# Kernel optimization log

Hardware: AMD Instinct MI355X
Metric: run time of the kernel (lower is better)

## Reference

```python
import jax, jax.numpy as jnp
import numpy as np

N, E, IN_FEATS, D, H, DIST_DIM, NBOUND = 10000, 160000, 128, 64, 4, 32, 31

def setup_inputs() -> dict:
    key = jax.random.key(0)
    ks = jax.random.split(key, 16)
    gain = 5.0 / 3.0  # tanh gain
    def xavier(k, shape):
        # xavier_normal over the last two dims (fan_in, fan_out) as torch does per-slice
        fan_in, fan_out = shape[-2], shape[-1]
        std = gain * np.sqrt(2.0 / (fan_in + fan_out))
        return jax.random.normal(k, shape, dtype=jnp.float32) * std
    inp = {
        'feat': jax.random.normal(ks[0], (N, IN_FEATS), dtype=jnp.float32),
        'locations': jax.random.normal(ks[1], (N, 3), dtype=jnp.float32),
        'src': jax.random.randint(ks[2], (E,), 0, N),
        'dst': jax.random.randint(ks[3], (E,), 0, N),
        'inter_ids': jax.random.randint(ks[4], (E, H), 0, N),
        'W_fc': xavier(ks[5], (IN_FEATS, H * D)),
        'embed_table': jax.random.normal(ks[6], (NBOUND + 1, DIST_DIM), dtype=jnp.float32),
        'G': xavier(ks[7], (H, DIST_DIM, D)),
        'attn_fc1': xavier(ks[8], (H, 2 * D, D)),
        'attn_fc2': xavier(ks[9], (H, 2 * D, D)),
        'attn_fc3': xavier(ks[10], (H, 2 * D, D)),
        'attn_fc': xavier(ks[11], (H, 3 * D, D)),
        'attn_out': xavier(ks[12], (H, D, 1)),
        'boundaries': jnp.linspace(0.1, 3.1, NBOUND).astype(jnp.float32),
    }
    return inp


def reference(feat, locations, W_fc, embed_table, G, attn_fc1, attn_fc2, attn_fc3,
              attn_fc, attn_out, boundaries, src, dst, inter_ids):
    n = feat.shape[0]
    h = (feat @ W_fc).reshape(n, H, D)                      # [N,H,D]
    pos = locations                                          # [N,3]
    src_pos = pos[src]                                       # [E,3]
    dst_pos = pos[dst]                                       # [E,3]
    inter_pos = pos[inter_ids]                               # [E,H,3]
    h_src = h[src]                                           # [E,H,D]
    h_dst = h[dst]                                           # [E,H,D]
    head_idx = jnp.arange(H)[None, :]
    inter_h = h[inter_ids, head_idx, :]                      # [E,H,D] per-head gather

    e_count = src.shape[0]
    dist1 = jnp.broadcast_to(jnp.linalg.norm(dst_pos - src_pos, axis=-1)[:, None], (e_count, H))
    dist2 = jnp.linalg.norm(dst_pos[:, None, :] - inter_pos, axis=-1)   # [E,H]
    dist_ = jnp.linalg.norm(src_pos[:, None, :] - inter_pos, axis=-1)   # [E,H]

    def dist_embed(dist):
        idx = jnp.searchsorted(boundaries, dist, side='left')  # torch.bucketize(right=False)
        e = embed_table[idx]                                   # [E,H,DIST_DIM]
        return jnp.einsum('ehk,hkd->ehd', e, G)                # [E,H,D]

    de1 = dist_embed(dist1)
    de2 = dist_embed(dist2)
    de_ = dist_embed(dist_)

    d1 = jnp.einsum('ehk,hkd->ehd', jnp.concatenate([h_src, de1], axis=-1), attn_fc1)
    d2 = jnp.einsum('ehk,hkd->ehd', jnp.concatenate([inter_h, de2], axis=-1), attn_fc2)
    d3 = jnp.einsum('ehk,hkd->ehd', jnp.concatenate([h_dst, de_], axis=-1), attn_fc3)

    h_c = jnp.tanh(jnp.einsum('ehk,hkd->ehd', jnp.concatenate([d1, d2, d3], axis=-1), attn_fc))
    e_score = jnp.einsum('ehd,hdo->eho', h_c, attn_out)[..., 0]        # [E,H]

    # edge softmax grouped by destination node
    m = jax.ops.segment_max(e_score, dst, num_segments=n)              # [N,H]
    ex = jnp.exp(e_score - m[dst])
    den = jax.ops.segment_sum(ex, dst, num_segments=n)                 # [N,H]
    a = ex / den[dst]                                                  # [E,H]

    ft = jax.ops.segment_sum(a[:, :, None] * h_src, dst, num_segments=n)  # [N,H,D]
    rst = jnp.mean(ft, axis=1)                                          # merge='mean' -> [N,D]
    return rst
```

## Files before the change

kernel.cpp:

```cpp
#include <hip/hip_runtime.h>
#include <hip/hip_fp16.h>
#include <math.h>

#define N_NODES 10000
#define E_EDGES 160000
#define DMODEL 64
#define H 4
#define NBOUND 31
#define SLOTS 64
#define QREC 1024

typedef _Float16 half8 __attribute__((ext_vector_type(8)));
typedef float floatx4 __attribute__((ext_vector_type(4)));

__device__ __forceinline__ void mm4(const float* __restrict__ S, int aoff,
                                    int astride, int boff, int i0, int j,
                                    int Kdim, float o[4]) {
  float a0 = 0.f, a1 = 0.f, a2 = 0.f, a3 = 0.f;
  for (int t4 = 0; t4 < (Kdim >> 2); ++t4) {
    float4 f0 = *(const float4*)&S[aoff + (i0 + 0) * astride + t4 * 4];
    float4 f1 = *(const float4*)&S[aoff + (i0 + 1) * astride + t4 * 4];
    float4 f2 = *(const float4*)&S[aoff + (i0 + 2) * astride + t4 * 4];
    float4 f3 = *(const float4*)&S[aoff + (i0 + 3) * astride + t4 * 4];
    float b0 = S[boff + (t4 * 4 + 0) * 64 + j];
    float b1 = S[boff + (t4 * 4 + 1) * 64 + j];
    float b2 = S[boff + (t4 * 4 + 2) * 64 + j];
    float b3 = S[boff + (t4 * 4 + 3) * 64 + j];
    a0 += f0.x * b0 + f0.y * b1 + f0.z * b2 + f0.w * b3;
    a1 += f1.x * b0 + f1.y * b1 + f1.z * b2 + f1.w * b3;
    a2 += f2.x * b0 + f2.y * b1 + f2.z * b2 + f2.w * b3;
    a3 += f3.x * b0 + f3.y * b1 + f3.z * b2 + f3.w * b3;
  }
  o[0] = a0; o[1] = a1; o[2] = a2; o[3] = a3;
}

__device__ __forceinline__ int didx(const float* __restrict__ bnd2, float d) {
  int g = (int)(d * 10.0f);
  g = (g < 0) ? 0 : ((g > 31) ? 31 : g);
  g += (bnd2[g + 1] < d) ? 1 : 0;
  g -= (bnd2[g] >= d) ? 1 : 0;
  return g;
}

__global__ __launch_bounds__(256) void edge_kernel(
    const float* __restrict__ pos, const int* __restrict__ src,
    const int* __restrict__ dst, const int* __restrict__ inter,
    const float* __restrict__ boundaries, int* __restrict__ cnt,
    uint4* __restrict__ ebuf) {
  __shared__ float Sb[48];
  int tid = threadIdx.x;
  if (tid < NBOUND) Sb[tid + 1] = boundaries[tid];
  if (tid == NBOUND) { Sb[0] = -INFINITY; Sb[32] = INFINITY; }
  __syncthreads();
  int e = blockIdx.x * 256 + tid;
  int s = src[e], t = dst[e];
  int4 iv = *(const int4*)&inter[e * 4];
  int itarr[4] = {iv.x, iv.y, iv.z, iv.w};
  float sx = pos[s * 3], sy = pos[s * 3 + 1], sz = pos[s * 3 + 2];
  float tx = pos[t * 3], ty = pos[t * 3 + 1], tz = pos[t * 3 + 2];
  float dx = tx - sx, dy = ty - sy, dz = tz - sz;
  float dist1 = sqrtf(dx * dx + dy * dy + dz * dz);
  unsigned i1 = (unsigned)didx(Sb, dist1);
  unsigned w3 = 0, q20 = 0, q_0 = 0;
  #pragma unroll
  for (int hh = 0; hh < 4; ++hh) {
    int it = itarr[hh];
    float ix = pos[it * 3], iy = pos[it * 3 + 1], iz = pos[it * 3 + 2];
    float ax = tx - ix, ay = ty - iy, az = tz - iz;
    float dist2 = sqrtf(ax * ax + ay * ay + az * az);
    float bx = sx - ix, by = sy - iy, bz = sz - iz;
    float dist_ = sqrtf(bx * bx + by * by + bz * bz);
    unsigned idx2 = (unsigned)didx(Sb, dist2);
    unsigned idx_ = (unsigned)didx(Sb, dist_);
    if (hh == 0) { q20 = idx2; q_0 = idx_; }
    else w3 |= (idx2 | (idx_ << 5)) << ((hh - 1) * 10);
  }
  uint4 rec;
  rec.x = (unsigned)s | ((unsigned)itarr[0] << 16);
  rec.y = (unsigned)itarr[1] | ((unsigned)itarr[2] << 16);
  rec.z = (unsigned)itarr[3] | (i1 << 16) | (q20 << 21) | (q_0 << 26);
  rec.w = w3;
  int p = atomicAdd(&cnt[t], 1);
  if (p < SLOTS) ebuf[t * SLOTS + p] = rec;
}

__global__ __launch_bounds__(256) void prep_kernel(
    const float* __restrict__ fc1, const float* __restrict__ fc2,
    const float* __restrict__ fc3, const float* __restrict__ fcc,
    const float* __restrict__ Wfc, const float* __restrict__ G,
    const float* __restrict__ emb, __half* __restrict__ bigWT,
    __half* __restrict__ U16) {
  __shared__ __align__(16) float S[12288];
  int bi = blockIdx.x;
  int tid = threadIdx.x;
  int k = bi >> 2, h = bi & 3;
  const float* fck = (k == 0) ? fc1 : (k == 1) ? fc2 : fc3;
  fck += h * 128 * 64;
  const float* F = fcc + h * 192 * 64 + k * 64 * 64;
  int j = tid & 63, ig = tid >> 6;
  float o[4];
  #pragma unroll
  for (int u = 0; u < 4; ++u) {
    ((float4*)S)[u * 256 + tid] = ((const float4*)F)[u * 256 + tid];
    ((float4*)(S + 4096))[u * 256 + tid] = ((const float4*)fck)[u * 256 + tid];
  }
  __syncthreads();
  #pragma unroll
  for (int rg = 0; rg < 4; ++rg) {
    int i0 = ig * 16 + rg * 4;
    mm4(S, 4096, 64, 0, i0, j, 64, o);
    S[8192 + (i0 + 0) * 64 + j] = o[0];
    S[8192 + (i0 + 1) * 64 + j] = o[1];
    S[8192 + (i0 + 2) * 64 + j] = o[2];
    S[8192 + (i0 + 3) * 64 + j] = o[3];
  }
  __syncthreads();
  #pragma unroll
  for (int u = 0; u < 4; ++u) {
    int fi = u * 256 + tid;
    int i = fi >> 4, c4 = fi & 15;
    ((float4*)(S + 4096))[fi] = ((const float4*)(Wfc + i * 256 + h * 64))[c4];
  }
  __syncthreads();
  if (k == 0) {
    #pragma unroll
    for (int u = 0; u < 16; ++u) {
      int idx = u * 256 + tid;
      int i = idx >> 6, jj = idx & 63;
      bigWT[(h * 64 + jj) * 128 + i] = __float2half(S[4096 + idx]);
    }
  }
  #pragma unroll
  for (int rg = 0; rg < 4; ++rg) {
    int i0 = ig * 16 + rg * 4;
    mm4(S, 4096, 64, 8192, i0, j, 64, o);
    int rb = ((k + 1) * 256 + h * 64 + j) * 128;
    bigWT[rb + i0 + 0] = __float2half(o[0]);
    bigWT[rb + i0 + 1] = __float2half(o[1]);
    bigWT[rb + i0 + 2] = __float2half(o[2]);
    bigWT[rb + i0 + 3] = __float2half(o[3]);
  }
  __syncthreads();
  #pragma unroll
  for (int u = 0; u < 4; ++u) {
    int fi = u * 256 + tid;
    int i = fi >> 4, c4 = fi & 15;
    ((float4*)(S + 4096))[fi] =
        ((const float4*)(Wfc + (64 + i) * 256 + h * 64))[c4];
  }
  __syncthreads();
  if (k == 0) {
    #pragma unroll
    for (int u = 0; u < 16; ++u) {
      int idx = u * 256 + tid;
      int i = idx >> 6, jj = idx & 63;
      bigWT[(h * 64 + jj) * 128 + 64 + i] = __float2half(S[4096 + idx]);
    }
  }
  #pragma unroll
  for (int rg = 0; rg < 4; ++rg) {
    int i0 = ig * 16 + rg * 4;
    mm4(S, 4096, 64, 8192, i0, j, 64, o);
    int rb = ((k + 1) * 256 + h * 64 + j) * 128;
    bigWT[rb + 64 + i0 + 0] = __float2half(o[0]);
    bigWT[rb + 64 + i0 + 1] = __float2half(o[1]);
    bigWT[rb + 64 + i0 + 2] = __float2half(o[2]);
    bigWT[rb + 64 + i0 + 3] = __float2half(o[3]);
  }
  __syncthreads();
  #pragma unroll
  for (int u = 0; u < 4; ++u)
    ((float4*)(S + 4096))[u * 256 + tid] =
        ((const float4*)(fck + 4096))[u * 256 + tid];
  __syncthreads();
  #pragma unroll
  for (int rg = 0; rg < 4; ++rg) {
    int i0 = ig * 16 + rg * 4;
    mm4(S, 4096, 64, 0, i0, j, 64, o);
    S[8192 + (i0 + 0) * 64 + j] = o[0];
    S[8192 + (i0 + 1) * 64 + j] = o[1];
    S[8192 + (i0 + 2) * 64 + j] = o[2];
    S[8192 + (i0 + 3) * 64 + j] = o[3];
  }
  __syncthreads();
  #pragma unroll
  for (int u = 0; u < 2; ++u)
    ((float4*)S)[u * 256 + tid] = ((const float4*)(G + h * 2048))[u * 256 + tid];
  ((float4*)(S + 2048))[tid] = ((const float4*)emb)[tid];
  __syncthreads();
  #pragma unroll
  for (int rg = 0; rg < 2; ++rg) {
    int i0 = ig * 8 + rg * 4;
    mm4(S, 0, 64, 8192, i0, j, 64, o);
    S[3072 + (i0 + 0) * 64 + j] = o[0];
    S[3072 + (i0 + 1) * 64 + j] = o[1];
    S[3072 + (i0 + 2) * 64 + j] = o[2];
    S[3072 + (i0 + 3) * 64 + j] = o[3];
  }
  __syncthreads();
  #pragma unroll
  for (int rg = 0; rg < 2; ++rg) {
    int i0 = ig * 8 + rg * 4;
    mm4(S, 2048, 32, 3072, i0, j, 32, o);
    int base = k * 8192 + h * 2048;
    U16[base + (i0 + 0) * 64 + j] = __float2half(o[0]);
    U16[base + (i0 + 1) * 64 + j] = __float2half(o[1]);
    U16[base + (i0 + 2) * 64 + j] = __float2half(o[2]);
    U16[base + (i0 + 3) * 64 + j] = __float2half(o[3]);
  }
}

#define EROW 264

__global__ __launch_bounds__(256) void gemm_kernel(
    const float* __restrict__ feat, const __half* __restrict__ bigWT,
    __half* __restrict__ qall) {
  __shared__ __align__(16) __half Esm[4][16][EROW];
  int bi = blockIdx.x;
  int tid = threadIdx.x;
  int bx = bi % 157, by = bi / 157;
  int wv = tid >> 6, l = tid & 63;
  int m0 = bx * 64 + wv * 16;
  int n0 = by * 256;
  int lm = l & 15, lk = (l >> 4) * 8;
  int arow = m0 + lm;
  if (arow >= N_NODES) arow = N_NODES - 1;
  const float* fp = feat + arow * 128 + lk;
  const _Float16* bp = (const _Float16*)bigWT + lk;
  half8 a[4];
  #pragma unroll
  for (int kt = 0; kt < 4; ++kt) {
    float4 u0 = *(const float4*)(fp + kt * 32);
    float4 u1 = *(const float4*)(fp + kt * 32 + 4);
    half8 t;
    t[0] = (_Float16)u0.x; t[1] = (_Float16)u0.y;
    t[2] = (_Float16)u0.z; t[3] = (_Float16)u0.w;
    t[4] = (_Float16)u1.x; t[5] = (_Float16)u1.y;
    t[6] = (_Float16)u1.z; t[7] = (_Float16)u1.w;
    a[kt] = t;
  }
  #pragma unroll
  for (int nt = 0; nt < 16; ++nt) {
    floatx4 acc = (floatx4){0.f, 0.f, 0.f, 0.f};
    #pragma unroll
    for (int kt = 0; kt < 4; ++kt) {
      half8 b = *(const half8*)(bp + (n0 + nt * 16 + lm) * 128 + kt * 32);
      acc = __builtin_amdgcn_mfma_f32_16x16x32_f16(a[kt], b, acc, 0, 0, 0);
    }
    int dd = nt * 16 + lm;
    int o = (by == 0) ? ((dd & 63) * 4 + (dd >> 6)) : dd;
    #pragma unroll
    for (int r4 = 0; r4 < 4; ++r4)
      Esm[wv][(l >> 4) * 4 + r4][o] = __float2half(acc[r4]);
  }
  __syncthreads();
  int row = l >> 2;
  int j0 = (l & 3) * 64;
  int m = m0 + row;
  if (m < N_NODES) {
    #pragma unroll
    for (int u = 0; u < 8; ++u) {
      uint4 v = *(const uint4*)&Esm[wv][row][j0 + u * 8];
      *(uint4*)&qall[m * QREC + by * 256 + j0 + u * 8] = v;
    }
  }
}

__device__ __forceinline__ float dpp_row_sum16(float v) {
  int x;
  x = __builtin_amdgcn_update_dpp(0, __float_as_int(v), 0x128, 0xf, 0xf, true);
  v += __int_as_float(x);
  x = __builtin_amdgcn_update_dpp(0, __float_as_int(v), 0x124, 0xf, 0xf, true);
  v += __int_as_float(x);
  x = __builtin_amdgcn_update_dpp(0, __float_as_int(v), 0x122, 0xf, 0xf, true);
  v += __int_as_float(x);
  x = __builtin_amdgcn_update_dpp(0, __float_as_int(v), 0x121, 0xf, 0xf, true);
  v += __int_as_float(x);
  return v;
}

union H4u { uint2 u; __half2 h[2]; };

__device__ __forceinline__ float tanh_dot(H4u A, H4u B, H4u C, H4u X, H4u Y,
                                          H4u Z, float4 a4) {
  __half2 z0 = __hadd2(__hadd2(A.h[0], B.h[0]), __hadd2(C.h[0], X.h[0]));
  z0 = __hadd2(z0, __hadd2(Y.h[0], Z.h[0]));
  __half2 z1 = __hadd2(__hadd2(A.h[1], B.h[1]), __hadd2(C.h[1], X.h[1]));
  z1 = __hadd2(z1, __hadd2(Y.h[1], Z.h[1]));
  float2 f0 = __half22float2(z0);
  float2 f1 = __half22float2(z1);
  const float K = 2.885390082f;
  float p0 = __builtin_amdgcn_exp2f(f0.x * K);
  float p1 = __builtin_amdgcn_exp2f(f0.y * K);
  float p2 = __builtin_amdgcn_exp2f(f1.x * K);
  float p3 = __builtin_amdgcn_exp2f(f1.y * K);
  float r0 = __builtin_amdgcn_rcpf(p0 + 1.0f);
  float r1 = __builtin_amdgcn_rcpf(p1 + 1.0f);
  float r2 = __builtin_amdgcn_rcpf(p2 + 1.0f);
  float r3 = __builtin_amdgcn_rcpf(p3 + 1.0f);
  float dot = a4.x * r0;
  dot = fmaf(a4.y, r1, dot);
  dot = fmaf(a4.z, r2, dot);
  dot = fmaf(a4.w, r3, dot);
  float asum = (a4.x + a4.y) + (a4.z + a4.w);
  return fmaf(-2.0f, dot, asum);
}

__device__ __forceinline__ float4 h4_to_f4(uint2 u) {
  union { uint2 ui; __half2 h[2]; } cc;
  cc.ui = u;
  float2 a = __half22float2(cc.h[0]);
  float2 b = __half22float2(cc.h[1]);
  return make_float4(a.x, a.y, b.x, b.y);
}

__device__ __forceinline__ void dec_rec(uint4 r, int h, int* s, int* it,
                                        unsigned* i1, unsigned* q2,
                                        unsigned* q_) {
  *s = (int)(r.x & 0xffff);
  *it = (h == 0) ? (int)(r.x >> 16)
      : (h == 1) ? (int)(r.y & 0xffff)
      : (h == 2) ? (int)(r.y >> 16) : (int)(r.z & 0xffff);
  *i1 = (r.z >> 16) & 31;
  if (h == 0) {
    *q2 = (r.z >> 21) & 31;
    *q_ = (r.z >> 26) & 31;
  } else {
    unsigned f = r.w >> ((h - 1) * 10);
    *q2 = f & 31;
    *q_ = (f >> 5) & 31;
  }
}

__device__ __forceinline__ void gather_edge(
    const __half* __restrict__ qall, const __half* __restrict__ U16, int h,
    int c, int lane, int s, int it, unsigned i1, unsigned q2, unsigned q_,
    H4u* A, H4u* B, H4u* X, H4u* Y, H4u* Z, uint2* hr) {
  A->u = *(const uint2*)(qall + s * QREC + 256 + h * 64 + c * 4);
  B->u = *(const uint2*)(qall + it * QREC + 512 + h * 64 + c * 4);
  X->u = *(const uint2*)(U16 + (h * 32 + (int)i1) * 64 + c * 4);
  Y->u = *(const uint2*)(U16 + 8192 + (h * 32 + (int)q2) * 64 + c * 4);
  Z->u = *(const uint2*)(U16 + 16384 + (h * 32 + (int)q_) * 64 + c * 4);
  *hr = *(const uint2*)(qall + s * QREC + lane * 4);
}

__global__ __launch_bounds__(256) void score_agg_kernel(
    const int* __restrict__ cnt, const uint4* __restrict__ ebuf,
    const __half* __restrict__ qall, const __half* __restrict__ U16,
    const float* __restrict__ aout, float* __restrict__ out) {
  __shared__ uint4 recs[SLOTS];
  __shared__ float4 sm_num[4][64];
  __shared__ float4 sm_den[4];
  int tid = threadIdx.x;
  int w = tid >> 6, lane = tid & 63;
  int h = lane >> 4, c = lane & 15;
  int n = blockIdx.x;
  int deg = cnt[n];
  if (deg > SLOTS) deg = SLOTS;
  if (tid < deg) recs[tid] = ebuf[n * SLOTS + tid];
  H4u C;
  C.u = *(const uint2*)(qall + n * QREC + 768 + h * 64 + c * 4);
  const float4 a4 = *((const float4*)(aout + h * 64) + c);
  __syncthreads();
  float4 num = make_float4(0.f, 0.f, 0.f, 0.f);
  float4 den = make_float4(0.f, 0.f, 0.f, 0.f);
  for (int i = w; i < deg; i += 8) {
    int iB = i + 4;
    int vB = (iB < deg);
    uint4 rA = recs[i];
    uint4 rB = recs[vB ? iB : i];
    int sA, itA, sB, itB;
    unsigned i1A, q2A, q_A, i1B, q2B, q_B;
    dec_rec(rA, h, &sA, &itA, &i1A, &q2A, &q_A);
    dec_rec(rB, h, &sB, &itB, &i1B, &q2B, &q_B);
    H4u A0, B0, X0, Y0, Z0, A1, B1, X1, Y1, Z1;
    uint2 hr0, hr1;
    gather_edge(qall, U16, h, c, lane, sA, itA, i1A, q2A, q_A, &A0, &B0, &X0,
                &Y0, &Z0, &hr0);
    gather_edge(qall, U16, h, c, lane, sB, itB, i1B, q2B, q_B, &A1, &B1, &X1,
                &Y1, &Z1, &hr1);
    float v0 = tanh_dot(A0, B0, C, X0, Y0, Z0, a4);
    float v1 = tanh_dot(A1, B1, C, X1, Y1, Z1, a4);
    v0 = dpp_row_sum16(v0);
    v1 = dpp_row_sum16(v1);
    float ex0 = __expf(v0);
    float ex1 = vB ? __expf(v1) : 0.f;
    float4 hv0 = h4_to_f4(hr0);
    float4 hv1 = h4_to_f4(hr1);
    float e00 = __shfl(ex0, 0), e01 = __shfl(ex0, 16);
    float e02 = __shfl(ex0, 32), e03 = __shfl(ex0, 48);
    float e10 = __shfl(ex1, 0), e11 = __shfl(ex1, 16);
    float e12 = __shfl(ex1, 32), e13 = __shfl(ex1, 48);
    num.x += e00 * hv0.x + e10 * hv1.x;
    num.y += e01 * hv0.y + e11 * hv1.y;
    num.z += e02 * hv0.z + e12 * hv1.z;
    num.w += e03 * hv0.w + e13 * hv1.w;
    den.x += e00 + e10;
    den.y += e01 + e11;
    den.z += e02 + e12;
    den.w += e03 + e13;
  }
  sm_num[w][lane] = num;
  if (lane == 0) sm_den[w] = den;
  __syncthreads();
  if (tid < 64) {
    float4 n0 = sm_num[0][tid], n1 = sm_num[1][tid];
    float4 n2 = sm_num[2][tid], n3 = sm_num[3][tid];
    float4 d0 = sm_den[0], d1 = sm_den[1], d2 = sm_den[2], d3 = sm_den[3];
    float4 ns = make_float4(n0.x + n1.x + n2.x + n3.x, n0.y + n1.y + n2.y + n3.y,
                            n0.z + n1.z + n2.z + n3.z, n0.w + n1.w + n2.w + n3.w);
    float4 ds = make_float4(d0.x + d1.x + d2.x + d3.x, d0.y + d1.y + d2.y + d3.y,
                            d0.z + d1.z + d2.z + d3.z, d0.w + d1.w + d2.w + d3.w);
    float r = 0.f;
    if (deg > 0)
      r = 0.25f * (ns.x / ds.x + ns.y / ds.y + ns.z / ds.z + ns.w / ds.w);
    out[n * 64 + tid] = r;
  }
}

extern "C" void kernel_launch(void* const* d_in, const int* in_sizes, int n_in,
                              void* d_out, int out_size, void* d_ws,
                              size_t ws_size, hipStream_t stream) {
  const float* feat = (const float*)d_in[0];
  const float* loc = (const float*)d_in[1];
  const int* src = (const int*)d_in[2];
  const int* dst = (const int*)d_in[3];
  const int* inter = (const int*)d_in[4];
  const float* Wfc = (const float*)d_in[5];
  const float* emb = (const float*)d_in[6];
  const float* G = (const float*)d_in[7];
  const float* fc1 = (const float*)d_in[8];
  const float* fc2 = (const float*)d_in[9];
  const float* fc3 = (const float*)d_in[10];
  const float* fcc = (const float*)d_in[11];
  const float* aout = (const float*)d_in[12];
  const float* bnd = (const float*)d_in[13];
  float* out = (float*)d_out;

  __half* qall = (__half*)d_ws;
  __half* bigWT = qall + N_NODES * QREC;
  __half* U16 = bigWT + 1024 * 128;
  uint4* ebuf = (uint4*)(U16 + 3 * H * 2048);
  int* cnt = (int*)(ebuf + N_NODES * SLOTS);

  hipMemsetAsync(cnt, 0, N_NODES * sizeof(int), stream);
  edge_kernel<<<E_EDGES / 256, 256, 0, stream>>>(loc, src, dst, inter, bnd,
                                                 cnt, ebuf);
  prep_kernel<<<12, 256, 0, stream>>>(fc1, fc2, fc3, fcc, Wfc, G, emb, bigWT,
                                      U16);
  gemm_kernel<<<628, 256, 0, stream>>>(feat, bigWT, qall);
  score_agg_kernel<<<N_NODES, 256, 0, stream>>>(cnt, ebuf, qall, U16, aout,
                                                out);
}
```

Measured before the change: 207.6 us.

## Map one node per wave in score_agg and split prep into parallel block chains

```diff
diff --git a/kernel.cpp b/kernel.cpp
--- a/kernel.cpp
+++ b/kernel.cpp
@@ -84,7 +84,7 @@
   if (p < SLOTS) ebuf[t * SLOTS + p] = rec;
 }
 
-__global__ __launch_bounds__(256) void prep_kernel(
+__global__ __launch_bounds__(512) void prep_kernel(
     const float* __restrict__ fc1, const float* __restrict__ fc2,
     const float* __restrict__ fc3, const float* __restrict__ fcc,
     const float* __restrict__ Wfc, const float* __restrict__ G,
@@ -93,21 +93,95 @@
   __shared__ __align__(16) float S[12288];
   int bi = blockIdx.x;
   int tid = threadIdx.x;
-  int k = bi >> 2, h = bi & 3;
+  int chain = (bi >= 12);
+  int kh = chain ? (bi - 12) : bi;
+  int k = kh >> 2, h = kh & 3;
   const float* fck = (k == 0) ? fc1 : (k == 1) ? fc2 : fc3;
   fck += h * 128 * 64;
   const float* F = fcc + h * 192 * 64 + k * 64 * 64;
   int j = tid & 63, ig = tid >> 6;
   float o[4];
+  if (!chain) {
+    #pragma unroll
+    for (int u = 0; u < 2; ++u) {
+      ((float4*)S)[u * 512 + tid] = ((const float4*)F)[u * 512 + tid];
+      ((float4*)(S + 4096))[u * 512 + tid] = ((const float4*)fck)[u * 512 + tid];
+    }
+    __syncthreads();
+    #pragma unroll
+    for (int rg = 0; rg < 2; ++rg) {
+      int i0 = ig * 8 + rg * 4;
+      mm4(S, 4096, 64, 0, i0, j, 64, o);
+      S[8192 + (i0 + 0) * 64 + j] = o[0];
+      S[8192 + (i0 + 1) * 64 + j] = o[1];
+      S[8192 + (i0 + 2) * 64 + j] = o[2];
+      S[8192 + (i0 + 3) * 64 + j] = o[3];
+    }
+    __syncthreads();
+    #pragma unroll
+    for (int u = 0; u < 2; ++u) {
+      int fi = u * 512 + tid;
+      int i = fi >> 4, c4 = fi & 15;
+      ((float4*)(S + 4096))[fi] = ((const float4*)(Wfc + i * 256 + h * 64))[c4];
+    }
+    __syncthreads();
+    if (k == 0) {
+      #pragma unroll
+      for (int u = 0; u < 8; ++u) {
+        int idx = u * 512 + tid;
+        int i = idx >> 6, jj = idx & 63;
+        bigWT[(h * 64 + jj) * 128 + i] = __float2half(S[4096 + idx]);
+      }
+    }
+    #pragma unroll
+    for (int rg = 0; rg < 2; ++rg) {
+      int i0 = ig * 8 + rg * 4;
+      mm4(S, 4096, 64, 8192, i0, j, 64, o);
+      int rb = ((k + 1) * 256 + h * 64 + j) * 128;
+      bigWT[rb + i0 + 0] = __float2half(o[0]);
+      bigWT[rb + i0 + 1] = __float2half(o[1]);
+      bigWT[rb + i0 + 2] = __float2half(o[2]);
+      bigWT[rb + i0 + 3] = __float2half(o[3]);
+    }
+    __syncthreads();
+    #pragma unroll
+    for (int u = 0; u < 2; ++u) {
+      int fi = u * 512 + tid;
+      int i = fi >> 4, c4 = fi & 15;
+      ((float4*)(S + 4096))[fi] =
+          ((const float4*)(Wfc + (64 + i) * 256 + h * 64))[c4];
+    }
+    __syncthreads();
+    if (k == 0) {
+      #pragma unroll
+      for (int u = 0; u < 8; ++u) {
+        int idx = u * 512 + tid;
+        int i = idx >> 6, jj = idx & 63;
+        bigWT[(h * 64 + jj) * 128 + 64 + i] = __float2half(S[4096 + idx]);
+      }
+    }
+    #pragma unroll
+    for (int rg = 0; rg < 2; ++rg) {
+      int i0 = ig * 8 + rg * 4;
+      mm4(S, 4096, 64, 8192, i0, j, 64, o);
+      int rb = ((k + 1) * 256 + h * 64 + j) * 128;
+      bigWT[rb + 64 + i0 + 0] = __float2half(o[0]);
+      bigWT[rb + 64 + i0 + 1] = __float2half(o[1]);
+      bigWT[rb + 64 + i0 + 2] = __float2half(o[2]);
+      bigWT[rb + 64 + i0 + 3] = __float2half(o[3]);
+    }
+    return;
+  }
   #pragma unroll
-  for (int u = 0; u < 4; ++u) {
-    ((float4*)S)[u * 256 + tid] = ((const float4*)F)[u * 256 + tid];
-    ((float4*)(S + 4096))[u * 256 + tid] = ((const float4*)fck)[u * 256 + tid];
+  for (int u = 0; u < 2; ++u) {
+    ((float4*)S)[u * 512 + tid] = ((const float4*)F)[u * 512 + tid];
+    ((float4*)(S + 4096))[u * 512 + tid] =
+        ((const float4*)(fck + 4096))[u * 512 + tid];
   }
   __syncthreads();
   #pragma unroll
-  for (int rg = 0; rg < 4; ++rg) {
-    int i0 = ig * 16 + rg * 4;
+  for (int rg = 0; rg < 2; ++rg) {
+    int i0 = ig * 8 + rg * 4;
     mm4(S, 4096, 64, 0, i0, j, 64, o);
     S[8192 + (i0 + 0) * 64 + j] = o[0];
     S[8192 + (i0 + 1) * 64 + j] = o[1];
@@ -115,82 +189,11 @@
     S[8192 + (i0 + 3) * 64 + j] = o[3];
   }
   __syncthreads();
-  #pragma unroll
-  for (int u = 0; u < 4; ++u) {
-    int fi = u * 256 + tid;
-    int i = fi >> 4, c4 = fi & 15;
-    ((float4*)(S + 4096))[fi] = ((const float4*)(Wfc + i * 256 + h * 64))[c4];
-  }
-  __syncthreads();
-  if (k == 0) {
-    #pragma unroll
-    for (int u = 0; u < 16; ++u) {
-      int idx = u * 256 + tid;
-      int i = idx >> 6, jj = idx & 63;
-      bigWT[(h * 64 + jj) * 128 + i] = __float2half(S[4096 + idx]);
-    }
-  }
-  #pragma unroll
-  for (int rg = 0; rg < 4; ++rg) {
-    int i0 = ig * 16 + rg * 4;
-    mm4(S, 4096, 64, 8192, i0, j, 64, o);
-    int rb = ((k + 1) * 256 + h * 64 + j) * 128;
-    bigWT[rb + i0 + 0] = __float2half(o[0]);
-    bigWT[rb + i0 + 1] = __float2half(o[1]);
-    bigWT[rb + i0 + 2] = __float2half(o[2]);
-    bigWT[rb + i0 + 3] = __float2half(o[3]);
-  }
-  __syncthreads();
-  #pragma unroll
-  for (int u = 0; u < 4; ++u) {
-    int fi = u * 256 + tid;
-    int i = fi >> 4, c4 = fi & 15;
-    ((float4*)(S + 4096))[fi] =
-        ((const float4*)(Wfc + (64 + i) * 256 + h * 64))[c4];
-  }
-  __syncthreads();
-  if (k == 0) {
-    #pragma unroll
-    for (int u = 0; u < 16; ++u) {
-      int idx = u * 256 + tid;
-      int i = idx >> 6, jj = idx & 63;
-      bigWT[(h * 64 + jj) * 128 + 64 + i] = __float2half(S[4096 + idx]);
-    }
-  }
-  #pragma unroll
-  for (int rg = 0; rg < 4; ++rg) {
-    int i0 = ig * 16 + rg * 4;
-    mm4(S, 4096, 64, 8192, i0, j, 64, o);
-    int rb = ((k + 1) * 256 + h * 64 + j) * 128;
-    bigWT[rb + 64 + i0 + 0] = __float2half(o[0]);
-    bigWT[rb + 64 + i0 + 1] = __float2half(o[1]);
-    bigWT[rb + 64 + i0 + 2] = __float2half(o[2]);
-    bigWT[rb + 64 + i0 + 3] = __float2half(o[3]);
-  }
-  __syncthreads();
-  #pragma unroll
-  for (int u = 0; u < 4; ++u)
-    ((float4*)(S + 4096))[u * 256 + tid] =
-        ((const float4*)(fck + 4096))[u * 256 + tid];
-  __syncthreads();
-  #pragma unroll
-  for (int rg = 0; rg < 4; ++rg) {
-    int i0 = ig * 16 + rg * 4;
-    mm4(S, 4096, 64, 0, i0, j, 64, o);
-    S[8192 + (i0 + 0) * 64 + j] = o[0];
-    S[8192 + (i0 + 1) * 64 + j] = o[1];
-    S[8192 + (i0 + 2) * 64 + j] = o[2];
-    S[8192 + (i0 + 3) * 64 + j] = o[3];
-  }
-  __syncthreads();
-  #pragma unroll
-  for (int u = 0; u < 2; ++u)
-    ((float4*)S)[u * 256 + tid] = ((const float4*)(G + h * 2048))[u * 256 + tid];
-  ((float4*)(S + 2048))[tid] = ((const float4*)emb)[tid];
-  __syncthreads();
-  #pragma unroll
-  for (int rg = 0; rg < 2; ++rg) {
-    int i0 = ig * 8 + rg * 4;
+  ((float4*)S)[tid] = ((const float4*)(G + h * 2048))[tid];
+  if (tid < 256) ((float4*)(S + 2048))[tid] = ((const float4*)emb)[tid];
+  __syncthreads();
+  {
+    int i0 = ig * 4;
     mm4(S, 0, 64, 8192, i0, j, 64, o);
     S[3072 + (i0 + 0) * 64 + j] = o[0];
     S[3072 + (i0 + 1) * 64 + j] = o[1];
@@ -198,9 +201,8 @@
     S[3072 + (i0 + 3) * 64 + j] = o[3];
   }
   __syncthreads();
-  #pragma unroll
-  for (int rg = 0; rg < 2; ++rg) {
-    int i0 = ig * 8 + rg * 4;
+  {
+    int i0 = ig * 4;
     mm4(S, 2048, 32, 3072, i0, j, 32, o);
     int base = k * 8192 + h * 2048;
     U16[base + (i0 + 0) * 64 + j] = __float2half(o[0]);
@@ -348,27 +350,25 @@
     const int* __restrict__ cnt, const uint4* __restrict__ ebuf,
     const __half* __restrict__ qall, const __half* __restrict__ U16,
     const float* __restrict__ aout, float* __restrict__ out) {
-  __shared__ uint4 recs[SLOTS];
-  __shared__ float4 sm_num[4][64];
-  __shared__ float4 sm_den[4];
+  __shared__ uint4 recs[4][SLOTS];
   int tid = threadIdx.x;
   int w = tid >> 6, lane = tid & 63;
   int h = lane >> 4, c = lane & 15;
-  int n = blockIdx.x;
+  int n = blockIdx.x * 4 + w;
   int deg = cnt[n];
   if (deg > SLOTS) deg = SLOTS;
-  if (tid < deg) recs[tid] = ebuf[n * SLOTS + tid];
+  if (lane < deg) recs[w][lane] = ebuf[n * SLOTS + lane];
   H4u C;
   C.u = *(const uint2*)(qall + n * QREC + 768 + h * 64 + c * 4);
   const float4 a4 = *((const float4*)(aout + h * 64) + c);
   __syncthreads();
   float4 num = make_float4(0.f, 0.f, 0.f, 0.f);
   float4 den = make_float4(0.f, 0.f, 0.f, 0.f);
-  for (int i = w; i < deg; i += 8) {
-    int iB = i + 4;
+  for (int i = 0; i < deg; i += 2) {
+    int iB = i + 1;
     int vB = (iB < deg);
-    uint4 rA = recs[i];
-    uint4 rB = recs[vB ? iB : i];
+    uint4 rA = recs[w][i];
+    uint4 rB = recs[w][vB ? iB : i];
     int sA, itA, sB, itB;
     unsigned i1A, q2A, q_A, i1B, q2B, q_B;
     dec_rec(rA, h, &sA, &itA, &i1A, &q2A, &q_A);
@@ -400,22 +400,10 @@
     den.z += e02 + e12;
     den.w += e03 + e13;
   }
-  sm_num[w][lane] = num;
-  if (lane == 0) sm_den[w] = den;
-  __syncthreads();
-  if (tid < 64) {
-    float4 n0 = sm_num[0][tid], n1 = sm_num[1][tid];
-    float4 n2 = sm_num[2][tid], n3 = sm_num[3][tid];
-    float4 d0 = sm_den[0], d1 = sm_den[1], d2 = sm_den[2], d3 = sm_den[3];
-    float4 ns = make_float4(n0.x + n1.x + n2.x + n3.x, n0.y + n1.y + n2.y + n3.y,
-                            n0.z + n1.z + n2.z + n3.z, n0.w + n1.w + n2.w + n3.w);
-    float4 ds = make_float4(d0.x + d1.x + d2.x + d3.x, d0.y + d1.y + d2.y + d3.y,
-                            d0.z + d1.z + d2.z + d3.z, d0.w + d1.w + d2.w + d3.w);
-    float r = 0.f;
-    if (deg > 0)
-      r = 0.25f * (ns.x / ds.x + ns.y / ds.y + ns.z / ds.z + ns.w / ds.w);
-    out[n * 64 + tid] = r;
-  }
+  float r = 0.f;
+  if (deg > 0)
+    r = 0.25f * (num.x / den.x + num.y / den.y + num.z / den.z + num.w / den.w);
+  out[n * 64 + lane] = r;
 }
 
 extern "C" void kernel_launch(void* const* d_in, const int* in_sizes, int n_in,
@@ -446,9 +434,9 @@
   hipMemsetAsync(cnt, 0, N_NODES * sizeof(int), stream);
   edge_kernel<<<E_EDGES / 256, 256, 0, stream>>>(loc, src, dst, inter, bnd,
                                                  cnt, ebuf);
-  prep_kernel<<<12, 256, 0, stream>>>(fc1, fc2, fc3, fcc, Wfc, G, emb, bigWT,
+  prep_kernel<<<24, 512, 0, stream>>>(fc1, fc2, fc3, fcc, Wfc, G, emb, bigWT,
                                       U16);
   gemm_kernel<<<628, 256, 0, stream>>>(feat, bigWT, qall);
-  score_agg_kernel<<<N_NODES, 256, 0, stream>>>(cnt, ebuf, qall, U16, aout,
-                                                out);
-}
+  score_agg_kernel<<<N_NODES / 4, 256, 0, stream>>>(cnt, ebuf, qall, U16, aout,
+                                                    out);
+}
```

After: 191.3 us. 7.8% less time.
